# Kernel optimization log

Hardware: AMD Instinct MI355X
Metric: run time of the kernel (lower is better)

The kernel has to match this reference:

```python
import jax, jax.numpy as jnp
import numpy as np

N, E, G = 50000, 1600000, 512
H, NF_IN, NF_OUT, GF_OUT, EDIM, DEPTH = 128, 64, 64, 128, 16, 3
EPS = 1e-5


def seg_softmax(logits, seg, num):
    m = jax.ops.segment_max(logits, seg, num_segments=num)
    e = jnp.exp(logits - m[seg])
    s = jax.ops.segment_sum(e, seg, num_segments=num)
    return e / s[seg]


def batchnorm_train(x, gamma, beta):
    mu = jnp.mean(x, axis=0)
    var = jnp.mean((x - mu) ** 2, axis=0)  # biased, as torch BN training
    return (x - mu) * jax.lax.rsqrt(var + EPS) * gamma + beta


def setup_inputs() -> dict:
    key = jax.random.key(0)
    ks = jax.random.split(key, 20)
    inp = {}
    inp['x'] = jax.random.normal(ks[0], (N, NF_IN), jnp.float32)
    inp['edge_index'] = jax.random.randint(ks[1], (2, E), 0, N, jnp.int64)
    inp['edge_attr'] = jax.random.normal(ks[2], (E, EDIM), jnp.float32)
    inp['batch'] = jnp.sort(jax.random.randint(ks[3], (N,), 0, G, jnp.int64))
    inp['num_graphs'] = G
    s = 0.05
    inp['Wi'] = jax.random.normal(ks[4], (H, NF_IN), jnp.float32) * s
    inp['bi'] = jnp.zeros((H,), jnp.float32)
    inp['gat_W'] = jax.random.normal(ks[5], (DEPTH, H, 2 * H), jnp.float32) * s
    inp['gat_a'] = jax.random.normal(ks[6], (DEPTH, 2 * H), jnp.float32) * s
    inp['nfW1'] = jax.random.normal(ks[7], (H, H), jnp.float32) * s
    inp['nfb1'] = jnp.zeros((H,), jnp.float32)
    inp['nf_g'] = jnp.ones((H,), jnp.float32)
    inp['nf_b'] = jnp.zeros((H,), jnp.float32)
    inp['nfW2'] = jax.random.normal(ks[8], (NF_OUT, H), jnp.float32) * s
    inp['nfb2'] = jnp.zeros((NF_OUT,), jnp.float32)
    inp['gfW1'] = jax.random.normal(ks[9], (H, H), jnp.float32) * s
    inp['gfb1'] = jnp.zeros((H,), jnp.float32)
    inp['gf_g'] = jnp.ones((H,), jnp.float32)
    inp['gf_b'] = jnp.zeros((H,), jnp.float32)
    inp['gfW2'] = jax.random.normal(ks[10], (GF_OUT, H), jnp.float32) * s
    inp['gfb2'] = jnp.zeros((GF_OUT,), jnp.float32)
    return inp


def reference(x, edge_index, edge_attr, batch, num_graphs, Wi, bi, gat_W, gat_a,
              nfW1, nfb1, nf_g, nf_b, nfW2, nfb2,
              gfW1, gfb1, gf_g, gf_b, gfW2, gfb2):
    src, dst = edge_index[0], edge_index[1]
    nf = x @ Wi.T + bi  # [N,H]
    for i in range(DEPTH):
        src_nf = nf[src]            # [E,H]
        dst_nf = nf[dst]            # [E,H]
        ef = jnp.concatenate([src_nf, dst_nf], axis=-1) @ gat_a[i]  # [E]
        alpha = seg_softmax(ef, dst, N)
        agg = jax.ops.segment_sum(alpha[:, None] * src_nf, dst, num_segments=N)
        nf = jax.nn.relu(jnp.concatenate([nf, agg], axis=-1) @ gat_W[i].T)
    # 3-iteration attention pooling over graphs
    h = nf
    for _ in range(3):
        logits = jnp.sum(h * nf, axis=-1)  # [N]
        alpha = seg_softmax(logits, batch, num_graphs)
        h = alpha[:, None] * nf
    gf = jax.ops.segment_sum(h, batch, num_segments=num_graphs)  # [G,H]
    nf_out = jax.nn.relu(batchnorm_train(nf @ nfW1.T + nfb1, nf_g, nf_b)) @ nfW2.T + nfb2
    gf_out = jax.nn.relu(batchnorm_train(gf @ gfW1.T + gfb1, gf_g, gf_b)) @ gfW2.T + gfb2
    return nf_out, edge_attr, gf_out
```

## Files before the change

kernel.cpp:

```cpp
#include <hip/hip_runtime.h>

#define NN 50000
#define NE 1600000
#define NG 512
#define HD 128
#define NGRP 8
#define GRPSZ ((NN + NGRP - 1) / NGRP)
#define PCAP 28672

typedef __attribute__((ext_vector_type(8))) short bf16x8;
typedef __attribute__((ext_vector_type(4))) float f32x4;

static __device__ __forceinline__ unsigned bf16rn(float x) {
  unsigned b = __float_as_uint(x);
  return (b + 0x7FFFu + ((b >> 16) & 1u)) >> 16;
}
static __device__ __forceinline__ float bf16tof(unsigned short u) {
  return __uint_as_float(((unsigned)u) << 16);
}

__global__ void __launch_bounds__(256) k_part(const int* __restrict__ src,
                                              const int* __restrict__ dst,
                                              uint2* __restrict__ pairs,
                                              int* __restrict__ pcnt) {
  __shared__ uint2 buf[8][512];
  __shared__ int lcnt[8];
  __shared__ int gbase[8];
  __shared__ int nfl[8];
  const int tid = threadIdx.x;
  const int b = blockIdx.x & 7;
  if (tid < 8) lcnt[tid] = 0;
  __syncthreads();
  const int stride = gridDim.x * 256;
  for (int base_e = blockIdx.x * 256; base_e < NE; base_e += stride) {
    int e = base_e + tid;
    bool valid = e < NE;
    if (valid) {
      int d = dst[e];
      int s = src[e];
      int g = d / GRPSZ;
      int pos = atomicAdd(&lcnt[g], 1);
      buf[g][pos] = make_uint2((unsigned)d, (unsigned)s);
    }
    __syncthreads();
    if (tid < 8) {
      int c = lcnt[tid];
      int nf = (c >= 256) ? 256 : 0;
      nfl[tid] = nf;
      gbase[tid] = nf ? atomicAdd(&pcnt[tid * 8 + b], nf) : 0;
    }
    __syncthreads();
#pragma unroll
    for (int g0 = 0; g0 < 8; ++g0) {
      if (nfl[g0]) {
        int gb = gbase[g0] + tid;
        if (gb < PCAP)
          pairs[(size_t)(g0 * 8 + b) * PCAP + gb] = buf[g0][tid];
      }
    }
    __syncthreads();
#pragma unroll
    for (int g0 = 0; g0 < 8; ++g0) {
      if (nfl[g0]) {
        int rem = lcnt[g0] - 256;
        if (tid < rem) buf[g0][tid] = buf[g0][256 + tid];
      }
    }
    __syncthreads();
    if (tid < 8 && nfl[tid]) lcnt[tid] -= 256;
    __syncthreads();
  }
  if (tid < 8) {
    int c = lcnt[tid];
    gbase[tid] = c ? atomicAdd(&pcnt[tid * 8 + b], c) : 0;
  }
  __syncthreads();
#pragma unroll
  for (int g0 = 0; g0 < 8; ++g0) {
    int c = lcnt[g0];
    if (tid < c) {
      int gb = gbase[g0] + tid;
      if (gb < PCAP)
        pairs[(size_t)(g0 * 8 + b) * PCAP + gb] = buf[g0][tid];
    }
  }
}

__global__ void __launch_bounds__(256) k_hist(const uint2* __restrict__ pairs,
                                              const int* __restrict__ pcnt,
                                              int* __restrict__ hcnt) {
  __shared__ int hist[GRPSZ];
  const int b = blockIdx.x;
  const int g = b & 7, sub = b >> 3;
  const int li = g * 8 + sub;
  const int lo = g * GRPSZ;
  for (int i = threadIdx.x; i < GRPSZ; i += 256) hist[i] = 0;
  __syncthreads();
  int cnt = min(pcnt[li], PCAP);
  const uint2* lst = pairs + (size_t)li * PCAP;
  for (int i = threadIdx.x; i < cnt; i += 256)
    atomicAdd(&hist[(int)lst[i].x - lo], 1);
  __syncthreads();
  for (int i = threadIdx.x; i < GRPSZ; i += 256)
    hcnt[(size_t)li * GRPSZ + i] = hist[i];
}

__global__ void __launch_bounds__(256) k_csr(const uint2* __restrict__ pairs,
                                             const int* __restrict__ pcnt,
                                             const int* __restrict__ hcnt,
                                             int* __restrict__ row_ptr,
                                             int* __restrict__ csr_src) {
  __shared__ int rp[GRPSZ];
  __shared__ int cur[GRPSZ];
  __shared__ int wsum[256];
  const int b = blockIdx.x;
  const int g = b & 7, sub = b >> 3;
  const int li = g * 8 + sub;
  const int lo = g * GRPSZ;
  int gbase = 0;
  for (int gg = 0; gg < g; ++gg)
#pragma unroll
    for (int ss = 0; ss < 8; ++ss) gbase += pcnt[gg * 8 + ss];
  for (int i = threadIdx.x; i < GRPSZ; i += 256) {
    int dsum = 0, before = 0;
#pragma unroll
    for (int ss = 0; ss < 8; ++ss) {
      int h = hcnt[(size_t)(g * 8 + ss) * GRPSZ + i];
      dsum += h;
      if (ss < sub) before += h;
    }
    rp[i] = dsum;
    cur[i] = before;
  }
  __syncthreads();
  const int CH = (GRPSZ + 255) / 256;
  int t0 = threadIdx.x * CH;
  int t1 = min(GRPSZ, t0 + CH);
  int s = 0;
  for (int i = t0; i < t1; ++i) { int v = rp[i]; rp[i] = s; s += v; }
  wsum[threadIdx.x] = s;
  __syncthreads();
  for (int off = 1; off < 256; off <<= 1) {
    int t = ((int)threadIdx.x >= off) ? wsum[threadIdx.x - off] : 0;
    __syncthreads();
    wsum[threadIdx.x] += t;
    __syncthreads();
  }
  int add = gbase + ((threadIdx.x > 0) ? wsum[threadIdx.x - 1] : 0);
  for (int i = t0; i < t1; ++i) rp[i] += add;
  __syncthreads();
  for (int i = threadIdx.x; i < GRPSZ; i += 256) {
    cur[i] += rp[i];
    if (sub == 0) row_ptr[lo + i] = rp[i];
  }
  if (sub == 0 && g == 7 && threadIdx.x == 0) row_ptr[NN] = NE;
  __syncthreads();
  int cnt = min(pcnt[li], PCAP);
  const uint2* lst = pairs + (size_t)li * PCAP;
  for (int i = threadIdx.x; i < cnt; i += 256) {
    uint2 p = lst[i];
    int pos = atomicAdd(&cur[(int)p.x - lo], 1);
    csr_src[pos] = (int)p.y;
  }
}

__global__ void k_init_bounds(int* __restrict__ gs, int* __restrict__ ge) {
  int g = blockIdx.x * 256 + threadIdx.x;
  if (g < NG) { gs[g] = NN; ge[g] = 0; }
}
__global__ void k_bounds(const int* __restrict__ batch, int* __restrict__ gs, int* __restrict__ ge) {
  int n = blockIdx.x * 256 + threadIdx.x;
  if (n < NN) {
    int b = batch[n];
    atomicMin(&gs[b], n);
    atomicMax(&ge[b], n + 1);
  }
}

__global__ void k_cvt3(const float* __restrict__ a0, int n0,
                       const float* __restrict__ a1, int n1,
                       const float* __restrict__ a2, int n2,
                       unsigned short* __restrict__ b) {
  int i = blockIdx.x * 256 + threadIdx.x;
  if (i >= n0 + n1 + n2) return;
  float v = (i < n0) ? a0[i] : (i < n0 + n1) ? a1[i - n0] : a2[i - n0 - n1];
  b[i] = (unsigned short)bf16rn(v);
}

template <bool LAST>
__global__ void __launch_bounds__(512) k_layer(
    const unsigned short* __restrict__ nf16, const uint4* __restrict__ nf16u4,
    const float* __restrict__ e1in,
    const int* __restrict__ row_ptr, const int* __restrict__ csr_src,
    const unsigned short* __restrict__ W16, const float* __restrict__ dvec,
    unsigned short* __restrict__ out16, float* __restrict__ dout) {
  __shared__ unsigned short aggl[64][136];
  __shared__ float pdot[64];
  const int tid = threadIdx.x;
  const int wid = tid >> 6;
  const int lane = tid & 63;
  const int row0 = blockIdx.x * 64;
  if (tid < 64) pdot[tid] = 0.f;

  {
    const int q = lane >> 3;
    const int c = lane & 7;
    for (int r = 0; r < 8; ++r) {
      const int slot = wid * 8 + r;
      const int node = row0 + slot;
      int s = 0, e = 0;
      if (node < NN) { s = row_ptr[node]; e = row_ptr[node + 1]; }
      float acc[16];
#pragma unroll
      for (int i = 0; i < 16; ++i) acc[i] = 0.f;
      float zloc = 0.f;
      int jj = s + q;
      bool v0 = jj < e;
      int sc = v0 ? csr_src[jj] : 0;
      float w = v0 ? e1in[sc] : 0.f;
      uint4 u0 = nf16u4[(size_t)sc * 16 + c * 2];
      uint4 u1 = nf16u4[(size_t)sc * 16 + c * 2 + 1];
      for (int j = s; j < e; j += 8) {
        int jn = j + 8 + q;
        bool vn = jn < e;
        int scn = vn ? csr_src[jn] : 0;
        float wn = vn ? e1in[scn] : 0.f;
        uint4 un0 = nf16u4[(size_t)scn * 16 + c * 2];
        uint4 un1 = nf16u4[(size_t)scn * 16 + c * 2 + 1];
        zloc += w;
        acc[0]  = fmaf(w, __uint_as_float(u0.x << 16), acc[0]);
        acc[1]  = fmaf(w, __uint_as_float(u0.x & 0xFFFF0000u), acc[1]);
        acc[2]  = fmaf(w, __uint_as_float(u0.y << 16), acc[2]);
        acc[3]  = fmaf(w, __uint_as_float(u0.y & 0xFFFF0000u), acc[3]);
        acc[4]  = fmaf(w, __uint_as_float(u0.z << 16), acc[4]);
        acc[5]  = fmaf(w, __uint_as_float(u0.z & 0xFFFF0000u), acc[5]);
        acc[6]  = fmaf(w, __uint_as_float(u0.w << 16), acc[6]);
        acc[7]  = fmaf(w, __uint_as_float(u0.w & 0xFFFF0000u), acc[7]);
        acc[8]  = fmaf(w, __uint_as_float(u1.x << 16), acc[8]);
        acc[9]  = fmaf(w, __uint_as_float(u1.x & 0xFFFF0000u), acc[9]);
        acc[10] = fmaf(w, __uint_as_float(u1.y << 16), acc[10]);
        acc[11] = fmaf(w, __uint_as_float(u1.y & 0xFFFF0000u), acc[11]);
        acc[12] = fmaf(w, __uint_as_float(u1.z << 16), acc[12]);
        acc[13] = fmaf(w, __uint_as_float(u1.z & 0xFFFF0000u), acc[13]);
        acc[14] = fmaf(w, __uint_as_float(u1.w << 16), acc[14]);
        acc[15] = fmaf(w, __uint_as_float(u1.w & 0xFFFF0000u), acc[15]);
        sc = scn; w = wn; u0 = un0; u1 = un1;
      }
      zloc += __shfl_xor(zloc, 8);
      zloc += __shfl_xor(zloc, 16);
      zloc += __shfl_xor(zloc, 32);
      float inv = (zloc > 0.f) ? 1.f / zloc : 0.f;
#pragma unroll
      for (int i = 0; i < 16; ++i) {
        acc[i] += __shfl_xor(acc[i], 8);
        acc[i] += __shfl_xor(acc[i], 16);
        acc[i] += __shfl_xor(acc[i], 32);
        acc[i] *= inv;
      }
      if (q == 0) {
        uint4 p0, p1;
        p0.x = bf16rn(acc[0])  | (bf16rn(acc[1])  << 16);
        p0.y = bf16rn(acc[2])  | (bf16rn(acc[3])  << 16);
        p0.z = bf16rn(acc[4])  | (bf16rn(acc[5])  << 16);
        p0.w = bf16rn(acc[6])  | (bf16rn(acc[7])  << 16);
        p1.x = bf16rn(acc[8])  | (bf16rn(acc[9])  << 16);
        p1.y = bf16rn(acc[10]) | (bf16rn(acc[11]) << 16);
        p1.z = bf16rn(acc[12]) | (bf16rn(acc[13]) << 16);
        p1.w = bf16rn(acc[14]) | (bf16rn(acc[15]) << 16);
        uint4* dst = (uint4*)(&aggl[slot][c * 16]);
        dst[0] = p0;
        dst[1] = p1;
      }
    }
  }
  __syncthreads();

  {
    const int lr = lane & 15;
    const int qq = lane >> 4;
    const int rblk = wid & 3, cblk = wid >> 2;
    const int rbase = row0 + rblk * 16;
    const int arow = min(rbase + lr, NN - 1);
    const unsigned short* pa1 = nf16 + (size_t)arow * 128;
    const unsigned short* pw = W16 + (size_t)(cblk * 64) * 256;

    f32x4 acc[4];
#pragma unroll
    for (int t = 0; t < 4; ++t) acc[t] = (f32x4){0.f, 0.f, 0.f, 0.f};

#pragma unroll
    for (int s = 0; s < 8; ++s) {
      bf16x8 af;
      if (s < 4) af = *(const bf16x8*)(pa1 + s * 32 + qq * 8);
      else       af = *(const bf16x8*)(&aggl[rblk * 16 + lr][(s - 4) * 32 + qq * 8]);
#pragma unroll
      for (int t = 0; t < 4; ++t) {
        bf16x8 bfr = *(const bf16x8*)(pw + (size_t)(t * 16 + lr) * 256 + s * 32 + qq * 8);
        acc[t] = __builtin_amdgcn_mfma_f32_16x16x32_bf16(af, bfr, acc[t], 0, 0, 0);
      }
    }

    float dv[4];
    if (!LAST) {
#pragma unroll
      for (int t = 0; t < 4; ++t) dv[t] = dvec[cblk * 64 + t * 16 + lr];
    }
    float p[4] = {0.f, 0.f, 0.f, 0.f};
#pragma unroll
    for (int j = 0; j < 4; ++j) {
      int n = rbase + qq * 4 + j;
      bool ok = n < NN;
#pragma unroll
      for (int t = 0; t < 4; ++t) {
        float v = fmaxf(acc[t][j], 0.f);
        if (ok) out16[(size_t)n * HD + cblk * 64 + t * 16 + lr] = (unsigned short)bf16rn(v);
        p[j] = fmaf(v, LAST ? v : dv[t], p[j]);
      }
      p[j] += __shfl_xor(p[j], 1);
      p[j] += __shfl_xor(p[j], 2);
      p[j] += __shfl_xor(p[j], 4);
      p[j] += __shfl_xor(p[j], 8);
    }
    if (lr == 0) {
#pragma unroll
      for (int j = 0; j < 4; ++j) atomicAdd(&pdot[rblk * 16 + qq * 4 + j], p[j]);
    }
  }
  __syncthreads();
  if (tid < 64) {
    int n = row0 + tid;
    if (n < NN) dout[n] = LAST ? pdot[tid] : __expf(pdot[tid]);
  }
}

template <int K, int KA, int HO, bool RELUOUT, bool BIAS, bool OUTF32, bool OUT16, int DOTM>
__global__ void __launch_bounds__(256) k_mfma(
    const unsigned short* __restrict__ A1, const unsigned short* __restrict__ A2,
    const unsigned short* __restrict__ W16, const float* __restrict__ bias,
    float* __restrict__ outf, unsigned short* __restrict__ out16,
    const float* __restrict__ dvec, float* __restrict__ dout, int nrows) {
  constexpr int NT = HO / 16;
  const int l = threadIdx.x & 63;
  const int w = threadIdx.x >> 6;
  const int lr = l & 15;
  const int q = l >> 4;
  const int row0 = blockIdx.x * 64 + w * 16;
  const int arow = min(row0 + lr, nrows - 1);
  const unsigned short* pa1 = A1 + (size_t)arow * KA;
  const unsigned short* pa2 = (KA < K) ? (A2 + (size_t)arow * (K - KA)) : nullptr;

  f32x4 acc[NT];
#pragma unroll
  for (int t = 0; t < NT; ++t) acc[t] = (f32x4){0.f, 0.f, 0.f, 0.f};

#pragma unroll
  for (int s = 0; s < K / 32; ++s) {
    const int kg = s * 32 + q * 8;
    bf16x8 af;
    if constexpr (KA == K) {
      af = *(const bf16x8*)(pa1 + kg);
    } else {
      af = (s * 32 < KA) ? *(const bf16x8*)(pa1 + kg)
                         : *(const bf16x8*)(pa2 + (kg - KA));
    }
#pragma unroll
    for (int t = 0; t < NT; ++t) {
      bf16x8 bfr = *(const bf16x8*)(W16 + (size_t)(t * 16 + lr) * K + kg);
      acc[t] = __builtin_amdgcn_mfma_f32_16x16x32_bf16(af, bfr, acc[t], 0, 0, 0);
    }
  }

  float bv[BIAS ? NT : 1];
  if constexpr (BIAS) {
#pragma unroll
    for (int t = 0; t < NT; ++t) bv[t] = bias[t * 16 + lr];
  }
  float dv[DOTM == 1 ? NT : 1];
  if constexpr (DOTM == 1) {
#pragma unroll
    for (int t = 0; t < NT; ++t) dv[t] = dvec[t * 16 + lr];
  }
  float p[4] = {0.f, 0.f, 0.f, 0.f};
#pragma unroll
  for (int j = 0; j < 4; ++j) {
    int n = row0 + q * 4 + j;
    bool ok = n < nrows;
#pragma unroll
    for (int t = 0; t < NT; ++t) {
      float v = acc[t][j];
      if constexpr (BIAS) v += bv[t];
      if constexpr (RELUOUT) v = fmaxf(v, 0.f);
      if (ok) {
        if constexpr (OUTF32) outf[(size_t)n * HO + t * 16 + lr] = v;
        if constexpr (OUT16) out16[(size_t)n * HO + t * 16 + lr] = (unsigned short)bf16rn(v);
      }
      if constexpr (DOTM == 1) p[j] = fmaf(v, dv[t], p[j]);
      if constexpr (DOTM == 2) p[j] = fmaf(v, v, p[j]);
    }
  }
  if constexpr (DOTM != 0) {
#pragma unroll
    for (int j = 0; j < 4; ++j) {
      p[j] += __shfl_xor(p[j], 1);
      p[j] += __shfl_xor(p[j], 2);
      p[j] += __shfl_xor(p[j], 4);
      p[j] += __shfl_xor(p[j], 8);
    }
    if (lr == 0) {
#pragma unroll
      for (int j = 0; j < 4; ++j) {
        int n = row0 + q * 4 + j;
        if (n < nrows) dout[n] = (DOTM == 1) ? __expf(p[j]) : p[j];
      }
    }
  }
}

template <int K, int KA, int HO, bool PRE, bool RELUOUT, bool BIAS, bool OUT16, int DOTM>
__global__ void __launch_bounds__(256) k_gemm(
    const float* __restrict__ inA, const float* __restrict__ inB,
    const float* __restrict__ W, const float* __restrict__ bias,
    const float* __restrict__ preA, const float* __restrict__ preB,
    float* __restrict__ out, int nrows,
    unsigned* __restrict__ out16, const float* __restrict__ dvec,
    float* __restrict__ dout) {
  constexpr int KC = 64;
  constexpr int BM = 64;
  constexpr int MT = 4;
  constexpr int NT = HO / 16;
  constexpr int LDW = HO + 4;
  constexpr int LDA = KC + 4;

  __shared__ float Wl[KC * LDW];
  __shared__ float inl[BM * LDA];

  const int tid = threadIdx.x;
  const int tr = tid >> 4;
  const int tc = tid & 15;
  const int row0 = blockIdx.x * BM;
  const int r0 = tr * MT;
  const int c0 = tc * NT;

  float acc[MT][NT];
#pragma unroll
  for (int i = 0; i < MT; ++i)
#pragma unroll
    for (int j = 0; j < NT; ++j) acc[i][j] = BIAS ? bias[c0 + j] : 0.f;

  for (int cc = 0; cc < K / KC; ++cc) {
    const int k0 = cc * KC;
    if (cc) __syncthreads();
    for (int idx = tid; idx < HO * (KC / 4); idx += 256) {
      int h = idx >> 4;
      int qq = idx & 15;
      float4 w = *(const float4*)(W + (size_t)h * K + k0 + qq * 4);
      Wl[(qq * 4 + 0) * LDW + h] = w.x;
      Wl[(qq * 4 + 1) * LDW + h] = w.y;
      Wl[(qq * 4 + 2) * LDW + h] = w.z;
      Wl[(qq * 4 + 3) * LDW + h] = w.w;
    }
    for (int idx = tid; idx < BM * (KC / 4); idx += 256) {
      int r = idx >> 4;
      int qq = idx & 15;
      int n = row0 + r;
      int kg = k0 + qq * 4;
      float4 v = make_float4(0.f, 0.f, 0.f, 0.f);
      if (n < nrows) {
        if constexpr (KA == K) {
          v = *(const float4*)(inA + (size_t)n * K + kg);
        } else {
          if (k0 < KA) v = *(const float4*)(inA + (size_t)n * KA + kg);
          else         v = *(const float4*)(inB + (size_t)n * (K - KA) + kg - KA);
        }
      }
      if constexpr (PRE) {
        v.x = fmaxf(v.x * preA[kg + 0] + preB[kg + 0], 0.f);
        v.y = fmaxf(v.y * preA[kg + 1] + preB[kg + 1], 0.f);
        v.z = fmaxf(v.z * preA[kg + 2] + preB[kg + 2], 0.f);
        v.w = fmaxf(v.w * preA[kg + 3] + preB[kg + 3], 0.f);
      }
      *(float4*)(inl + r * LDA + qq * 4) = v;
    }
    __syncthreads();
#pragma unroll 8
    for (int k = 0; k < KC; ++k) {
      float a[MT];
#pragma unroll
      for (int i = 0; i < MT; ++i) a[i] = inl[(r0 + i) * LDA + k];
      float4 b0 = *(const float4*)(Wl + k * LDW + c0);
#pragma unroll
      for (int i = 0; i < MT; ++i) {
        acc[i][0] = fmaf(a[i], b0.x, acc[i][0]);
        acc[i][1] = fmaf(a[i], b0.y, acc[i][1]);
        acc[i][2] = fmaf(a[i], b0.z, acc[i][2]);
        acc[i][3] = fmaf(a[i], b0.w, acc[i][3]);
      }
      if constexpr (NT == 8) {
        float4 b1 = *(const float4*)(Wl + k * LDW + c0 + 4);
#pragma unroll
        for (int i = 0; i < MT; ++i) {
          acc[i][4] = fmaf(a[i], b1.x, acc[i][4]);
          acc[i][5] = fmaf(a[i], b1.y, acc[i][5]);
          acc[i][6] = fmaf(a[i], b1.z, acc[i][6]);
          acc[i][7] = fmaf(a[i], b1.w, acc[i][7]);
        }
      }
    }
  }
  float dv[DOTM == 1 ? NT : 1];
  if constexpr (DOTM == 1) {
#pragma unroll
    for (int j = 0; j < NT; ++j) dv[j] = dvec[c0 + j];
  }
#pragma unroll
  for (int i = 0; i < MT; ++i) {
    int n = row0 + r0 + i;
    if constexpr (RELUOUT) {
#pragma unroll
      for (int j = 0; j < NT; ++j) acc[i][j] = fmaxf(acc[i][j], 0.f);
    }
    if (n < nrows) {
      float4 o0 = make_float4(acc[i][0], acc[i][1], acc[i][2], acc[i][3]);
      *(float4*)(out + (size_t)n * HO + c0) = o0;
      if constexpr (NT == 8) {
        float4 o1 = make_float4(acc[i][4], acc[i][5], acc[i][6], acc[i][7]);
        *(float4*)(out + (size_t)n * HO + c0 + 4) = o1;
      }
      if constexpr (OUT16 && NT == 8) {
        uint4 pk;
        pk.x = bf16rn(acc[i][0]) | (bf16rn(acc[i][1]) << 16);
        pk.y = bf16rn(acc[i][2]) | (bf16rn(acc[i][3]) << 16);
        pk.z = bf16rn(acc[i][4]) | (bf16rn(acc[i][5]) << 16);
        pk.w = bf16rn(acc[i][6]) | (bf16rn(acc[i][7]) << 16);
        *(uint4*)(out16 + (size_t)n * 64 + tc * 4) = pk;
      }
    }
    if constexpr (DOTM != 0) {
      float p = 0.f;
#pragma unroll
      for (int j = 0; j < NT; ++j)
        p = fmaf(acc[i][j], (DOTM == 1) ? dv[j] : acc[i][j], p);
      p += __shfl_xor(p, 1);
      p += __shfl_xor(p, 2);
      p += __shfl_xor(p, 4);
      p += __shfl_xor(p, 8);
      if (tc == 0 && n < nrows) dout[n] = (DOTM == 1) ? __expf(p) : p;
    }
  }
}

__global__ void k_pool(const unsigned short* __restrict__ nf16, const float* __restrict__ r,
                       const int* __restrict__ gs, const int* __restrict__ ge,
                       float* __restrict__ alpha, float* __restrict__ gf) {
  int g = blockIdx.x;
  int s = gs[g], e = ge[g];
  __shared__ float red[256];
  for (int it = 0; it < 3; ++it) {
    float lm = -INFINITY;
    for (int n = s + threadIdx.x; n < e; n += 256) {
      float l = r[n];
      if (it) l *= alpha[n];
      lm = fmaxf(lm, l);
    }
    red[threadIdx.x] = lm;
    __syncthreads();
    for (int off = 128; off > 0; off >>= 1) {
      if ((int)threadIdx.x < off) red[threadIdx.x] = fmaxf(red[threadIdx.x], red[threadIdx.x + off]);
      __syncthreads();
    }
    float m = red[0];
    __syncthreads();
    float zz = 0.f;
    for (int n = s + threadIdx.x; n < e; n += 256) {
      float l = r[n];
      if (it) l *= alpha[n];
      zz += __expf(l - m);
    }
    red[threadIdx.x] = zz;
    __syncthreads();
    for (int off = 128; off > 0; off >>= 1) {
      if ((int)threadIdx.x < off) red[threadIdx.x] += red[threadIdx.x + off];
      __syncthreads();
    }
    float z = red[0];
    __syncthreads();
    float invz = 1.f / z;
    for (int n = s + threadIdx.x; n < e; n += 256) {
      float l = r[n];
      if (it) l *= alpha[n];
      alpha[n] = __expf(l - m) * invz;
    }
    __syncthreads();
  }
  int c = threadIdx.x & 127;
  int rr2 = threadIdx.x >> 7;
  float acc = 0.f;
  for (int n = s + rr2; n < e; n += 2)
    acc += alpha[n] * bf16tof(nf16[(size_t)n * HD + c]);
  red[threadIdx.x] = acc;
  __syncthreads();
  if (rr2 == 0) gf[(size_t)g * HD + c] = red[threadIdx.x] + red[threadIdx.x + 128];
}

__global__ void k_colstats(const float* __restrict__ y, float* __restrict__ sum,
                           float* __restrict__ sumsq, int R, int CH) {
  int c = threadIdx.x & 127;
  int rr = threadIdx.x >> 7;
  int r0 = blockIdx.x * CH;
  int r1 = min(R, r0 + CH);
  float s = 0.f, q = 0.f;
  for (int r = r0 + rr; r < r1; r += 2) {
    float v = y[(size_t)r * HD + c];
    s += v;
    q += v * v;
  }
  __shared__ float ls[256], lq[256];
  ls[threadIdx.x] = s;
  lq[threadIdx.x] = q;
  __syncthreads();
  if (rr == 0) {
    s += ls[threadIdx.x + 128];
    q += lq[threadIdx.x + 128];
    atomicAdd(&sum[c], s);
    atomicAdd(&sumsq[c], q);
  }
}

__global__ void k_bn_final(const float* __restrict__ sum, const float* __restrict__ sumsq,
                           const float* __restrict__ g, const float* __restrict__ b,
                           float* __restrict__ A, float* __restrict__ B, float R) {
  int c = threadIdx.x;
  float mu = sum[c] / R;
  float var = sumsq[c] / R - mu * mu;
  float a = g[c] * rsqrtf(var + 1e-5f);
  A[c] = a;
  B[c] = b[c] - mu * a;
}

__global__ void k_bnapply(const float* __restrict__ y, const float* __restrict__ Ac,
                          const float* __restrict__ Bc, unsigned short* __restrict__ z) {
  int i = blockIdx.x * 256 + threadIdx.x;
  if (i >= NN * 16) return;
  int c = (i & 15) * 8;
  const float4* yp = (const float4*)y + (size_t)i * 2;
  float4 v0 = yp[0], v1 = yp[1];
  float4 a0 = *(const float4*)(Ac + c), a1 = *(const float4*)(Ac + c + 4);
  float4 b0 = *(const float4*)(Bc + c), b1 = *(const float4*)(Bc + c + 4);
  float r0 = fmaxf(fmaf(v0.x, a0.x, b0.x), 0.f);
  float r1 = fmaxf(fmaf(v0.y, a0.y, b0.y), 0.f);
  float r2 = fmaxf(fmaf(v0.z, a0.z, b0.z), 0.f);
  float r3 = fmaxf(fmaf(v0.w, a0.w, b0.w), 0.f);
  float r4 = fmaxf(fmaf(v1.x, a1.x, b1.x), 0.f);
  float r5 = fmaxf(fmaf(v1.y, a1.y, b1.y), 0.f);
  float r6 = fmaxf(fmaf(v1.z, a1.z, b1.z), 0.f);
  float r7 = fmaxf(fmaf(v1.w, a1.w, b1.w), 0.f);
  uint4 pk;
  pk.x = bf16rn(r0) | (bf16rn(r1) << 16);
  pk.y = bf16rn(r2) | (bf16rn(r3) << 16);
  pk.z = bf16rn(r4) | (bf16rn(r5) << 16);
  pk.w = bf16rn(r6) | (bf16rn(r7) << 16);
  *(uint4*)(z + (size_t)i * 8) = pk;
}

__global__ void k_copy4(const float4* __restrict__ a, float4* __restrict__ b, int n) {
  int i = blockIdx.x * 256 + threadIdx.x;
  if (i < n) b[i] = a[i];
}

extern "C" void kernel_launch(void* const* d_in, const int* in_sizes, int n_in,
                              void* d_out, int out_size, void* d_ws, size_t ws_size,
                              hipStream_t stream) {
  const float* x        = (const float*)d_in[0];
  const int*   ei       = (const int*)d_in[1];
  const float* edge_attr= (const float*)d_in[2];
  const int*   batch    = (const int*)d_in[3];
  const float* Wi       = (const float*)d_in[5];
  const float* bi       = (const float*)d_in[6];
  const float* gat_W    = (const float*)d_in[7];
  const float* gat_a    = (const float*)d_in[8];
  const float* nfW1     = (const float*)d_in[9];
  const float* nfb1     = (const float*)d_in[10];
  const float* nf_g     = (const float*)d_in[11];
  const float* nf_b     = (const float*)d_in[12];
  const float* nfW2     = (const float*)d_in[13];
  const float* nfb2     = (const float*)d_in[14];
  const float* gfW1     = (const float*)d_in[15];
  const float* gfb1     = (const float*)d_in[16];
  const float* gf_g     = (const float*)d_in[17];
  const float* gf_b     = (const float*)d_in[18];
  const float* gfW2     = (const float*)d_in[19];
  const float* gfb2     = (const float*)d_in[20];

  float* out = (float*)d_out;

  unsigned short* nf16A = (unsigned short*)d_ws;
  unsigned short* nf16B = nf16A + (size_t)NN * HD;
  unsigned short* z16   = nf16B + (size_t)NN * HD;
  unsigned short* wt_gat = z16 + (size_t)NN * HD;
  unsigned short* wt_nf1 = wt_gat + 3 * 128 * 256;
  unsigned short* wt_nf2 = wt_nf1 + 128 * 128;
  float* nfA   = (float*)(wt_nf2 + 64 * 128);
  float* e1A   = nfA + (size_t)NN * HD;
  float* e1B   = e1A + NN;
  float* rv    = e1B + NN;
  float* alpha = rv + NN;
  float* gf    = alpha + NN;
  float* gy    = gf + (size_t)NG * HD;
  int*   pcnt  = (int*)(gy + (size_t)NG * HD);
  float* sums  = (float*)(pcnt + 64);
  float* sums2 = sums + 256;
  float* bnAB  = sums2 + 256;
  int* row_ptr = (int*)(bnAB + 256);
  int* csr_src = row_ptr + NN + 1;
  int* gs      = csr_src + NE;
  int* ge      = gs + NG;
  int* hcnt    = ge + NG;
  uint2* pairs = (uint2*)nfA;

  const int* src  = ei;
  const int* dstp = ei + NE;

  hipMemsetAsync(pcnt, 0, (64 + 512) * sizeof(int), stream);

  k_part<<<512, 256, 0, stream>>>(src, dstp, pairs, pcnt);
  k_hist<<<64, 256, 0, stream>>>(pairs, pcnt, hcnt);
  k_csr<<<64, 256, 0, stream>>>(pairs, pcnt, hcnt, row_ptr, csr_src);

  k_init_bounds<<<2, 256, 0, stream>>>(gs, ge);
  k_bounds<<<(NN + 255) / 256, 256, 0, stream>>>(batch, gs, ge);

  k_cvt3<<<(3 * 128 * 256 + 128 * 128 + 64 * 128 + 255) / 256, 256, 0, stream>>>(
      gat_W, 3 * 128 * 256, nfW1, 128 * 128, nfW2, 64 * 128, wt_gat);

  k_gemm<64, 64, 128, false, false, true, true, 1><<<(NN + 63) / 64, 256, 0, stream>>>(
      x, nullptr, Wi, bi, nullptr, nullptr, nfA, NN, (unsigned*)nf16A, gat_a, e1A);

  const int layer_grid = (NN + 63) / 64;
  k_layer<false><<<layer_grid, 512, 0, stream>>>(
      nf16A, (const uint4*)nf16A, e1A, row_ptr, csr_src,
      wt_gat + 0 * 128 * 256, gat_a + 1 * 256, nf16B, e1B);
  k_layer<false><<<layer_grid, 512, 0, stream>>>(
      nf16B, (const uint4*)nf16B, e1B, row_ptr, csr_src,
      wt_gat + 1 * 128 * 256, gat_a + 2 * 256, nf16A, e1A);
  k_layer<true><<<layer_grid, 512, 0, stream>>>(
      nf16A, (const uint4*)nf16A, e1A, row_ptr, csr_src,
      wt_gat + 2 * 128 * 256, nullptr, nf16B, rv);
  unsigned short* cur = nf16B;

  k_pool<<<NG, 256, 0, stream>>>(cur, rv, gs, ge, alpha, gf);

  const int gemm_grid = (NN + 63) / 64;
  k_mfma<128, 128, 128, false, true, true, false, 0><<<gemm_grid, 256, 0, stream>>>(
      cur, nullptr, wt_nf1, nfb1, nfA, nullptr, nullptr, nullptr, NN);
  k_colstats<<<200, 256, 0, stream>>>(nfA, sums, sums + 128, NN, 250);
  k_bn_final<<<1, 128, 0, stream>>>(sums, sums + 128, nf_g, nf_b, bnAB, bnAB + 128, (float)NN);
  k_bnapply<<<(NN * 16 + 255) / 256, 256, 0, stream>>>(nfA, bnAB, bnAB + 128, z16);
  k_mfma<128, 128, 64, false, true, true, false, 0><<<gemm_grid, 256, 0, stream>>>(
      z16, nullptr, wt_nf2, nfb2, out, nullptr, nullptr, nullptr, NN);

  k_gemm<128, 128, 128, false, false, true, false, 0><<<(NG + 63) / 64, 256, 0, stream>>>(
      gf, nullptr, gfW1, gfb1, nullptr, nullptr, gy, NG, nullptr, nullptr, nullptr);
  k_colstats<<<4, 256, 0, stream>>>(gy, sums2, sums2 + 128, NG, 128);
  k_bn_final<<<1, 128, 0, stream>>>(sums2, sums2 + 128, gf_g, gf_b, bnAB, bnAB + 128, (float)NG);
  k_gemm<128, 128, 128, true, false, true, false, 0><<<(NG + 63) / 64, 256, 0, stream>>>(
      gy, nullptr, gfW2, gfb2, bnAB, bnAB + 128,
      out + (size_t)NN * 64 + (size_t)NE * 16, NG, nullptr, nullptr, nullptr);

  int n4 = NE * 16 / 4;
  k_copy4<<<(n4 + 255) / 256, 256, 0, stream>>>((const float4*)edge_attr,
                                                (float4*)(out + (size_t)NN * 64), n4);
}
```

Before: 635.7 us.

## Fuse BN statistics into head GEMM and BN-apply into second GEMM

The node-head pipeline drops its separate column-statistics and BN-apply kernels. The first head GEMM now accumulates per-column sum and sum of squares in its epilogue, via shared-memory then global atomics. The second GEMM applies the BN affine, ReLU and bf16 conversion while loading its A operand, so the z16 intermediate buffer is gone. The aim is to cut two full passes over the 50k×128 float activations plus launch overhead, at the cost of atomic contention and a dependency on the stat buffers being zeroed. Separately, the GAT gather loop now fetches edge source indices two iterations ahead to hide the index-load latency behind the feature loads.

```diff
diff --git a/kernel.cpp b/kernel.cpp
--- a/kernel.cpp
+++ b/kernel.cpp
@@ -214,37 +214,36 @@
 #pragma unroll
       for (int i = 0; i < 16; ++i) acc[i] = 0.f;
       float zloc = 0.f;
-      int jj = s + q;
-      bool v0 = jj < e;
-      int sc = v0 ? csr_src[jj] : 0;
-      float w = v0 ? e1in[sc] : 0.f;
-      uint4 u0 = nf16u4[(size_t)sc * 16 + c * 2];
-      uint4 u1 = nf16u4[(size_t)sc * 16 + c * 2 + 1];
+      int j0 = s + q;      bool p0 = j0 < e;  int sc0 = p0 ? csr_src[j0] : 0;
+      int j1 = s + 8 + q;  bool p1 = j1 < e;  int sc1 = p1 ? csr_src[j1] : 0;
+      float w0 = p0 ? e1in[sc0] : 0.f;
+      uint4 a0 = nf16u4[(size_t)sc0 * 16 + c * 2];
+      uint4 a1 = nf16u4[(size_t)sc0 * 16 + c * 2 + 1];
       for (int j = s; j < e; j += 8) {
-        int jn = j + 8 + q;
-        bool vn = jn < e;
-        int scn = vn ? csr_src[jn] : 0;
-        float wn = vn ? e1in[scn] : 0.f;
-        uint4 un0 = nf16u4[(size_t)scn * 16 + c * 2];
-        uint4 un1 = nf16u4[(size_t)scn * 16 + c * 2 + 1];
-        zloc += w;
-        acc[0]  = fmaf(w, __uint_as_float(u0.x << 16), acc[0]);
-        acc[1]  = fmaf(w, __uint_as_float(u0.x & 0xFFFF0000u), acc[1]);
-        acc[2]  = fmaf(w, __uint_as_float(u0.y << 16), acc[2]);
-        acc[3]  = fmaf(w, __uint_as_float(u0.y & 0xFFFF0000u), acc[3]);
-        acc[4]  = fmaf(w, __uint_as_float(u0.z << 16), acc[4]);
-        acc[5]  = fmaf(w, __uint_as_float(u0.z & 0xFFFF0000u), acc[5]);
-        acc[6]  = fmaf(w, __uint_as_float(u0.w << 16), acc[6]);
-        acc[7]  = fmaf(w, __uint_as_float(u0.w & 0xFFFF0000u), acc[7]);
-        acc[8]  = fmaf(w, __uint_as_float(u1.x << 16), acc[8]);
-        acc[9]  = fmaf(w, __uint_as_float(u1.x & 0xFFFF0000u), acc[9]);
-        acc[10] = fmaf(w, __uint_as_float(u1.y << 16), acc[10]);
-        acc[11] = fmaf(w, __uint_as_float(u1.y & 0xFFFF0000u), acc[11]);
-        acc[12] = fmaf(w, __uint_as_float(u1.z << 16), acc[12]);
-        acc[13] = fmaf(w, __uint_as_float(u1.z & 0xFFFF0000u), acc[13]);
-        acc[14] = fmaf(w, __uint_as_float(u1.w << 16), acc[14]);
-        acc[15] = fmaf(w, __uint_as_float(u1.w & 0xFFFF0000u), acc[15]);
-        sc = scn; w = wn; u0 = un0; u1 = un1;
+        int j2 = j + 16 + q; bool p2 = j2 < e;
+        int sc2 = p2 ? csr_src[j2] : 0;
+        float w1 = p1 ? e1in[sc1] : 0.f;
+        uint4 b0 = nf16u4[(size_t)sc1 * 16 + c * 2];
+        uint4 b1 = nf16u4[(size_t)sc1 * 16 + c * 2 + 1];
+        zloc += w0;
+        acc[0]  = fmaf(w0, __uint_as_float(a0.x << 16), acc[0]);
+        acc[1]  = fmaf(w0, __uint_as_float(a0.x & 0xFFFF0000u), acc[1]);
+        acc[2]  = fmaf(w0, __uint_as_float(a0.y << 16), acc[2]);
+        acc[3]  = fmaf(w0, __uint_as_float(a0.y & 0xFFFF0000u), acc[3]);
+        acc[4]  = fmaf(w0, __uint_as_float(a0.z << 16), acc[4]);
+        acc[5]  = fmaf(w0, __uint_as_float(a0.z & 0xFFFF0000u), acc[5]);
+        acc[6]  = fmaf(w0, __uint_as_float(a0.w << 16), acc[6]);
+        acc[7]  = fmaf(w0, __uint_as_float(a0.w & 0xFFFF0000u), acc[7]);
+        acc[8]  = fmaf(w0, __uint_as_float(a1.x << 16), acc[8]);
+        acc[9]  = fmaf(w0, __uint_as_float(a1.x & 0xFFFF0000u), acc[9]);
+        acc[10] = fmaf(w0, __uint_as_float(a1.y << 16), acc[10]);
+        acc[11] = fmaf(w0, __uint_as_float(a1.y & 0xFFFF0000u), acc[11]);
+        acc[12] = fmaf(w0, __uint_as_float(a1.z << 16), acc[12]);
+        acc[13] = fmaf(w0, __uint_as_float(a1.z & 0xFFFF0000u), acc[13]);
+        acc[14] = fmaf(w0, __uint_as_float(a1.w << 16), acc[14]);
+        acc[15] = fmaf(w0, __uint_as_float(a1.w & 0xFFFF0000u), acc[15]);
+        w0 = w1; a0 = b0; a1 = b1;
+        sc1 = sc2; p1 = p2;
       }
       zloc += __shfl_xor(zloc, 8);
       zloc += __shfl_xor(zloc, 16);
@@ -258,18 +257,18 @@
         acc[i] *= inv;
       }
       if (q == 0) {
-        uint4 p0, p1;
-        p0.x = bf16rn(acc[0])  | (bf16rn(acc[1])  << 16);
-        p0.y = bf16rn(acc[2])  | (bf16rn(acc[3])  << 16);
-        p0.z = bf16rn(acc[4])  | (bf16rn(acc[5])  << 16);
-        p0.w = bf16rn(acc[6])  | (bf16rn(acc[7])  << 16);
-        p1.x = bf16rn(acc[8])  | (bf16rn(acc[9])  << 16);
-        p1.y = bf16rn(acc[10]) | (bf16rn(acc[11]) << 16);
-        p1.z = bf16rn(acc[12]) | (bf16rn(acc[13]) << 16);
-        p1.w = bf16rn(acc[14]) | (bf16rn(acc[15]) << 16);
+        uint4 p0k, p1k;
+        p0k.x = bf16rn(acc[0])  | (bf16rn(acc[1])  << 16);
+        p0k.y = bf16rn(acc[2])  | (bf16rn(acc[3])  << 16);
+        p0k.z = bf16rn(acc[4])  | (bf16rn(acc[5])  << 16);
+        p0k.w = bf16rn(acc[6])  | (bf16rn(acc[7])  << 16);
+        p1k.x = bf16rn(acc[8])  | (bf16rn(acc[9])  << 16);
+        p1k.y = bf16rn(acc[10]) | (bf16rn(acc[11]) << 16);
+        p1k.z = bf16rn(acc[12]) | (bf16rn(acc[13]) << 16);
+        p1k.w = bf16rn(acc[14]) | (bf16rn(acc[15]) << 16);
         uint4* dst = (uint4*)(&aggl[slot][c * 16]);
-        dst[0] = p0;
-        dst[1] = p1;
+        dst[0] = p0k;
+        dst[1] = p1k;
       }
     }
   }
@@ -333,85 +332,123 @@
   }
 }
 
-template <int K, int KA, int HO, bool RELUOUT, bool BIAS, bool OUTF32, bool OUT16, int DOTM>
-__global__ void __launch_bounds__(256) k_mfma(
-    const unsigned short* __restrict__ A1, const unsigned short* __restrict__ A2,
-    const unsigned short* __restrict__ W16, const float* __restrict__ bias,
-    float* __restrict__ outf, unsigned short* __restrict__ out16,
-    const float* __restrict__ dvec, float* __restrict__ dout, int nrows) {
-  constexpr int NT = HO / 16;
+__global__ void __launch_bounds__(256) k_head1(
+    const unsigned short* __restrict__ A1, const unsigned short* __restrict__ W16,
+    const float* __restrict__ bias, float* __restrict__ outf,
+    float* __restrict__ statS, float* __restrict__ statQ) {
+  __shared__ float bs[128], bq[128];
   const int l = threadIdx.x & 63;
   const int w = threadIdx.x >> 6;
   const int lr = l & 15;
   const int q = l >> 4;
   const int row0 = blockIdx.x * 64 + w * 16;
-  const int arow = min(row0 + lr, nrows - 1);
-  const unsigned short* pa1 = A1 + (size_t)arow * KA;
-  const unsigned short* pa2 = (KA < K) ? (A2 + (size_t)arow * (K - KA)) : nullptr;
-
-  f32x4 acc[NT];
-#pragma unroll
-  for (int t = 0; t < NT; ++t) acc[t] = (f32x4){0.f, 0.f, 0.f, 0.f};
-
-#pragma unroll
-  for (int s = 0; s < K / 32; ++s) {
-    const int kg = s * 32 + q * 8;
-    bf16x8 af;
-    if constexpr (KA == K) {
-      af = *(const bf16x8*)(pa1 + kg);
-    } else {
-      af = (s * 32 < KA) ? *(const bf16x8*)(pa1 + kg)
-                         : *(const bf16x8*)(pa2 + (kg - KA));
-    }
-#pragma unroll
-    for (int t = 0; t < NT; ++t) {
-      bf16x8 bfr = *(const bf16x8*)(W16 + (size_t)(t * 16 + lr) * K + kg);
+  const int arow = min(row0 + lr, NN - 1);
+  const unsigned short* pa1 = A1 + (size_t)arow * 128;
+  if (threadIdx.x < 128) { bs[threadIdx.x] = 0.f; bq[threadIdx.x] = 0.f; }
+
+  f32x4 acc[8];
+#pragma unroll
+  for (int t = 0; t < 8; ++t) acc[t] = (f32x4){0.f, 0.f, 0.f, 0.f};
+#pragma unroll
+  for (int s = 0; s < 4; ++s) {
+    bf16x8 af = *(const bf16x8*)(pa1 + s * 32 + q * 8);
+#pragma unroll
+    for (int t = 0; t < 8; ++t) {
+      bf16x8 bfr = *(const bf16x8*)(W16 + (size_t)(t * 16 + lr) * 128 + s * 32 + q * 8);
       acc[t] = __builtin_amdgcn_mfma_f32_16x16x32_bf16(af, bfr, acc[t], 0, 0, 0);
     }
   }
-
-  float bv[BIAS ? NT : 1];
-  if constexpr (BIAS) {
-#pragma unroll
-    for (int t = 0; t < NT; ++t) bv[t] = bias[t * 16 + lr];
-  }
-  float dv[DOTM == 1 ? NT : 1];
-  if constexpr (DOTM == 1) {
-#pragma unroll
-    for (int t = 0; t < NT; ++t) dv[t] = dvec[t * 16 + lr];
-  }
-  float p[4] = {0.f, 0.f, 0.f, 0.f};
+  float bv[8];
+#pragma unroll
+  for (int t = 0; t < 8; ++t) bv[t] = bias[t * 16 + lr];
+  float ps[8], pq[8];
+#pragma unroll
+  for (int t = 0; t < 8; ++t) { ps[t] = 0.f; pq[t] = 0.f; }
 #pragma unroll
   for (int j = 0; j < 4; ++j) {
     int n = row0 + q * 4 + j;
-    bool ok = n < nrows;
-#pragma unroll
-    for (int t = 0; t < NT; ++t) {
-      float v = acc[t][j];
-      if constexpr (BIAS) v += bv[t];
-      if constexpr (RELUOUT) v = fmaxf(v, 0.f);
+    bool ok = n < NN;
+#pragma unroll
+    for (int t = 0; t < 8; ++t) {
+      float v = acc[t][j] + bv[t];
       if (ok) {
-        if constexpr (OUTF32) outf[(size_t)n * HO + t * 16 + lr] = v;
-        if constexpr (OUT16) out16[(size_t)n * HO + t * 16 + lr] = (unsigned short)bf16rn(v);
-      }
-      if constexpr (DOTM == 1) p[j] = fmaf(v, dv[t], p[j]);
-      if constexpr (DOTM == 2) p[j] = fmaf(v, v, p[j]);
-    }
-  }
-  if constexpr (DOTM != 0) {
-#pragma unroll
-    for (int j = 0; j < 4; ++j) {
-      p[j] += __shfl_xor(p[j], 1);
-      p[j] += __shfl_xor(p[j], 2);
-      p[j] += __shfl_xor(p[j], 4);
-      p[j] += __shfl_xor(p[j], 8);
-    }
-    if (lr == 0) {
-#pragma unroll
-      for (int j = 0; j < 4; ++j) {
-        int n = row0 + q * 4 + j;
-        if (n < nrows) dout[n] = (DOTM == 1) ? __expf(p[j]) : p[j];
-      }
+        outf[(size_t)n * HD + t * 16 + lr] = v;
+        ps[t] += v;
+        pq[t] += v * v;
+      }
+    }
+  }
+  __syncthreads();
+#pragma unroll
+  for (int t = 0; t < 8; ++t) {
+    ps[t] += __shfl_xor(ps[t], 16);
+    ps[t] += __shfl_xor(ps[t], 32);
+    pq[t] += __shfl_xor(pq[t], 16);
+    pq[t] += __shfl_xor(pq[t], 32);
+  }
+  if (q == 0) {
+#pragma unroll
+    for (int t = 0; t < 8; ++t) {
+      atomicAdd(&bs[t * 16 + lr], ps[t]);
+      atomicAdd(&bq[t * 16 + lr], pq[t]);
+    }
+  }
+  __syncthreads();
+  if (threadIdx.x < 128) {
+    atomicAdd(&statS[threadIdx.x], bs[threadIdx.x]);
+    atomicAdd(&statQ[threadIdx.x], bq[threadIdx.x]);
+  }
+}
+
+__global__ void __launch_bounds__(256) k_head2(
+    const float* __restrict__ y, const unsigned short* __restrict__ W16,
+    const float* __restrict__ bnA, const float* __restrict__ bnB,
+    const float* __restrict__ bias, float* __restrict__ outf) {
+  const int l = threadIdx.x & 63;
+  const int w = threadIdx.x >> 6;
+  const int lr = l & 15;
+  const int q = l >> 4;
+  const int row0 = blockIdx.x * 64 + w * 16;
+  const int arow = min(row0 + lr, NN - 1);
+  const float* py = y + (size_t)arow * 128;
+
+  f32x4 acc[4];
+#pragma unroll
+  for (int t = 0; t < 4; ++t) acc[t] = (f32x4){0.f, 0.f, 0.f, 0.f};
+#pragma unroll
+  for (int s = 0; s < 4; ++s) {
+    const int kg = s * 32 + q * 8;
+    float4 y0 = *(const float4*)(py + kg);
+    float4 y1 = *(const float4*)(py + kg + 4);
+    float4 A0 = *(const float4*)(bnA + kg);
+    float4 A1v = *(const float4*)(bnA + kg + 4);
+    float4 B0 = *(const float4*)(bnB + kg);
+    float4 B1v = *(const float4*)(bnB + kg + 4);
+    bf16x8 af;
+    af[0] = (short)bf16rn(fmaxf(fmaf(y0.x, A0.x, B0.x), 0.f));
+    af[1] = (short)bf16rn(fmaxf(fmaf(y0.y, A0.y, B0.y), 0.f));
+    af[2] = (short)bf16rn(fmaxf(fmaf(y0.z, A0.z, B0.z), 0.f));
+    af[3] = (short)bf16rn(fmaxf(fmaf(y0.w, A0.w, B0.w), 0.f));
+    af[4] = (short)bf16rn(fmaxf(fmaf(y1.x, A1v.x, B1v.x), 0.f));
+    af[5] = (short)bf16rn(fmaxf(fmaf(y1.y, A1v.y, B1v.y), 0.f));
+    af[6] = (short)bf16rn(fmaxf(fmaf(y1.z, A1v.z, B1v.z), 0.f));
+    af[7] = (short)bf16rn(fmaxf(fmaf(y1.w, A1v.w, B1v.w), 0.f));
+#pragma unroll
+    for (int t = 0; t < 4; ++t) {
+      bf16x8 bfr = *(const bf16x8*)(W16 + (size_t)(t * 16 + lr) * 128 + kg);
+      acc[t] = __builtin_amdgcn_mfma_f32_16x16x32_bf16(af, bfr, acc[t], 0, 0, 0);
+    }
+  }
+  float bv[4];
+#pragma unroll
+  for (int t = 0; t < 4; ++t) bv[t] = bias[t * 16 + lr];
+#pragma unroll
+  for (int j = 0; j < 4; ++j) {
+    int n = row0 + q * 4 + j;
+    if (n < NN) {
+#pragma unroll
+      for (int t = 0; t < 4; ++t)
+        outf[(size_t)n * 64 + t * 16 + lr] = acc[t][j] + bv[t];
     }
   }
 }
@@ -635,31 +672,6 @@
   float a = g[c] * rsqrtf(var + 1e-5f);
   A[c] = a;
   B[c] = b[c] - mu * a;
-}
-
-__global__ void k_bnapply(const float* __restrict__ y, const float* __restrict__ Ac,
-                          const float* __restrict__ Bc, unsigned short* __restrict__ z) {
-  int i = blockIdx.x * 256 + threadIdx.x;
-  if (i >= NN * 16) return;
-  int c = (i & 15) * 8;
-  const float4* yp = (const float4*)y + (size_t)i * 2;
-  float4 v0 = yp[0], v1 = yp[1];
-  float4 a0 = *(const float4*)(Ac + c), a1 = *(const float4*)(Ac + c + 4);
-  float4 b0 = *(const float4*)(Bc + c), b1 = *(const float4*)(Bc + c + 4);
-  float r0 = fmaxf(fmaf(v0.x, a0.x, b0.x), 0.f);
-  float r1 = fmaxf(fmaf(v0.y, a0.y, b0.y), 0.f);
-  float r2 = fmaxf(fmaf(v0.z, a0.z, b0.z), 0.f);
-  float r3 = fmaxf(fmaf(v0.w, a0.w, b0.w), 0.f);
-  float r4 = fmaxf(fmaf(v1.x, a1.x, b1.x), 0.f);
-  float r5 = fmaxf(fmaf(v1.y, a1.y, b1.y), 0.f);
-  float r6 = fmaxf(fmaf(v1.z, a1.z, b1.z), 0.f);
-  float r7 = fmaxf(fmaf(v1.w, a1.w, b1.w), 0.f);
-  uint4 pk;
-  pk.x = bf16rn(r0) | (bf16rn(r1) << 16);
-  pk.y = bf16rn(r2) | (bf16rn(r3) << 16);
-  pk.z = bf16rn(r4) | (bf16rn(r5) << 16);
-  pk.w = bf16rn(r6) | (bf16rn(r7) << 16);
-  *(uint4*)(z + (size_t)i * 8) = pk;
 }
 
 __global__ void k_copy4(const float4* __restrict__ a, float4* __restrict__ b, int n) {
@@ -695,8 +707,7 @@
 
   unsigned short* nf16A = (unsigned short*)d_ws;
   unsigned short* nf16B = nf16A + (size_t)NN * HD;
-  unsigned short* z16   = nf16B + (size_t)NN * HD;
-  unsigned short* wt_gat = z16 + (size_t)NN * HD;
+  unsigned short* wt_gat = nf16B + (size_t)NN * HD;
   unsigned short* wt_nf1 = wt_gat + 3 * 128 * 256;
   unsigned short* wt_nf2 = wt_nf1 + 128 * 128;
   float* nfA   = (float*)(wt_nf2 + 64 * 128);
@@ -750,13 +761,9 @@
   k_pool<<<NG, 256, 0, stream>>>(cur, rv, gs, ge, alpha, gf);
 
   const int gemm_grid = (NN + 63) / 64;
-  k_mfma<128, 128, 128, false, true, true, false, 0><<<gemm_grid, 256, 0, stream>>>(
-      cur, nullptr, wt_nf1, nfb1, nfA, nullptr, nullptr, nullptr, NN);
-  k_colstats<<<200, 256, 0, stream>>>(nfA, sums, sums + 128, NN, 250);
+  k_head1<<<gemm_grid, 256, 0, stream>>>(cur, wt_nf1, nfb1, nfA, sums, sums + 128);
   k_bn_final<<<1, 128, 0, stream>>>(sums, sums + 128, nf_g, nf_b, bnAB, bnAB + 128, (float)NN);
-  k_bnapply<<<(NN * 16 + 255) / 256, 256, 0, stream>>>(nfA, bnAB, bnAB + 128, z16);
-  k_mfma<128, 128, 64, false, true, true, false, 0><<<gemm_grid, 256, 0, stream>>>(
-      z16, nullptr, wt_nf2, nfb2, out, nullptr, nullptr, nullptr, NN);
+  k_head2<<<gemm_grid, 256, 0, stream>>>(nfA, wt_nf2, bnAB, bnAB + 128, nfb2, out);
 
   k_gemm<128, 128, 128, false, false, true, false, 0><<<(NG + 63) / 64, 256, 0, stream>>>(
       gf, nullptr, gfW1, gfb1, nullptr, nullptr, gy, NG, nullptr, nullptr, nullptr);
```

Result: faster. 613.0 us (-3.6%).
